# Kernel tuning notes

Hardware: AMD Instinct MI355X
Metric: run time of the kernel (lower is better)

## Reference

```python
import jax, jax.numpy as jnp
import numpy as np

B, N, D = 4, 2048, 1024

def setup_inputs() -> dict:
    key = jax.random.key(0)
    ks = jax.random.split(key, 8)
    s = 1.0 / np.sqrt(D)
    return {
        "x": jax.random.normal(ks[0], (B, N, D), dtype=jnp.float32),
        "Wq": jax.random.normal(ks[1], (D, D), dtype=jnp.float32) * s,
        "bq": jnp.zeros((D,), dtype=jnp.float32),
        "Wk": jax.random.normal(ks[2], (D, D), dtype=jnp.float32) * s,
        "bk": jnp.zeros((D,), dtype=jnp.float32),
        "Wv": jax.random.normal(ks[3], (D, D), dtype=jnp.float32) * s,
        "bv": jnp.zeros((D,), dtype=jnp.float32),
        "gamma": jnp.ones((1,), dtype=jnp.float32),
    }

def reference(x, Wq, bq, Wk, bk, Wv, bv, gamma):
    d = x.shape[-1]
    delta = 1.0 / jnp.sqrt(jnp.asarray(d, dtype=x.dtype))
    # torch Linear: y = x @ W.T + b, W is [out, in]
    Q = jnp.einsum('bnd,ed->bne', x, Wq) + bq
    K = jnp.einsum('bnd,ed->bne', x, Wk) + bk
    V = jnp.einsum('bnd,ed->bne', x, Wv) + bv
    scores = jnp.einsum('bne,bme->bnm', Q, K) * delta  # [B, N, N]
    attn = jax.nn.softmax(scores, axis=-1)
    out = jnp.einsum('bnm,bme->bne', attn, V)
    return out * gamma + x
```

## Files before the change

kernel.cpp:

```cpp
#include <hip/hip_runtime.h>

typedef _Float16 f16;
typedef __attribute__((ext_vector_type(4))) _Float16 f16x4;
typedef __attribute__((ext_vector_type(8))) _Float16 f16x8;
typedef __attribute__((ext_vector_type(4))) float f32x4;

#define B_ 4
#define N_ 2048
#define D_ 1024

__global__ __launch_bounds__(256) void k_cast_all(const float4* __restrict__ x,
                                                  const float4* __restrict__ wq,
                                                  const float4* __restrict__ wk,
                                                  const float4* __restrict__ wv,
                                                  f16x4* __restrict__ xo,
                                                  f16x4* __restrict__ wqo,
                                                  f16x4* __restrict__ wko,
                                                  f16x4* __restrict__ wvo) {
  int b = blockIdx.x;
  const float4* in;
  f16x4* out;
  int idx;
  if (b < 8192)       { in = x;  out = xo;  idx = b * 256 + threadIdx.x; }
  else if (b < 9216)  { in = wq; out = wqo; idx = (b - 8192) * 256 + threadIdx.x; }
  else if (b < 10240) { in = wk; out = wko; idx = (b - 9216) * 256 + threadIdx.x; }
  else                { in = wv; out = wvo; idx = (b - 10240) * 256 + threadIdx.x; }
  float4 v = in[idx];
  f16x4 o = { (_Float16)v.x, (_Float16)v.y, (_Float16)v.z, (_Float16)v.w };
  out[idx] = o;
}

__device__ __forceinline__ void stage_tile(const char* gRowBase, int rowStrideBytes,
                                           int kByte, char* lds, int tid) {
#pragma unroll
  for (int it = 0; it < 4; ++it) {
    int lin = it * 4096 + tid * 16;
    int row = lin >> 7;
    int pchunk = (lin >> 4) & 7;
    int lchunk = pchunk ^ (row & 7);
    const char* g = gRowBase + (long)row * rowStrideBytes + kByte + lchunk * 16;
    char* l = lds + it * 4096 + ((tid >> 6) << 10);
    __builtin_amdgcn_global_load_lds(
        (const __attribute__((address_space(1))) unsigned int*)g,
        (__attribute__((address_space(3))) unsigned int*)l, 16, 0, 0);
  }
}

__device__ __forceinline__ void gemm_mainloop(const f16* __restrict__ A, int lda,
                                              const f16* __restrict__ B, int ldb,
                                              int K, char* ldsA, char* ldsB,
                                              f32x4 acc[4][4]) {
  const int tid = threadIdx.x;
  const int lane = tid & 63, wave = tid >> 6;
  const int wm = wave >> 1, wn = wave & 1;
  const int quad = lane >> 4, l16 = lane & 15;
  const char* Ab = (const char*)A;
  const char* Bb = (const char*)B;
  const int nK = K >> 6;
  for (int ks = 0; ks < nK; ++ks) {
    __syncthreads();
    stage_tile(Ab, lda * 2, ks * 128, ldsA, tid);
    stage_tile(Bb, ldb * 2, ks * 128, ldsB, tid);
    __syncthreads();
#pragma unroll
    for (int kk = 0; kk < 2; ++kk) {
      f16x8 af[4], bfv[4];
#pragma unroll
      for (int i = 0; i < 4; ++i) {
        int c = kk * 4 + quad;
        int rA = wm * 64 + i * 16 + l16;
        af[i] = *(const f16x8*)(ldsA + rA * 128 + ((c ^ (rA & 7)) << 4));
        int rB = wn * 64 + i * 16 + l16;
        bfv[i] = *(const f16x8*)(ldsB + rB * 128 + ((c ^ (rB & 7)) << 4));
      }
#pragma unroll
      for (int i = 0; i < 4; ++i)
#pragma unroll
        for (int j = 0; j < 4; ++j)
          acc[i][j] = __builtin_amdgcn_mfma_f32_16x16x32_f16(af[i], bfv[j], acc[i][j], 0, 0, 0);
    }
  }
}

__global__ __launch_bounds__(256, 2) void k_qkv(const f16* __restrict__ X,
                                                const f16* __restrict__ Wq,
                                                const f16* __restrict__ Wk,
                                                const f16* __restrict__ Wv,
                                                const float* __restrict__ bq,
                                                const float* __restrict__ bk,
                                                const float* __restrict__ bv,
                                                f16* __restrict__ Q, f16* __restrict__ Ko,
                                                f16* __restrict__ V) {
  __shared__ __align__(16) char ldsX[16384];
  __shared__ __align__(16) char ldsW[3][16384];
  int tm = blockIdx.y * 128, tn = blockIdx.x * 128;
  const int tid = threadIdx.x;
  const int lane = tid & 63, wave = tid >> 6;
  const int wm = wave >> 1, wn = wave & 1;
  const int quad = lane >> 4, l16 = lane & 15;
  f32x4 acc[3][4][4];
#pragma unroll
  for (int w = 0; w < 3; ++w)
#pragma unroll
    for (int i = 0; i < 4; ++i)
#pragma unroll
      for (int j = 0; j < 4; ++j) acc[w][i][j] = (f32x4){0.f, 0.f, 0.f, 0.f};

  const char* Xb = (const char*)(X + (long)tm * D_);
  const char* Wb[3] = { (const char*)(Wq + (long)tn * D_),
                        (const char*)(Wk + (long)tn * D_),
                        (const char*)(Wv + (long)tn * D_) };
  for (int ks = 0; ks < (D_ >> 6); ++ks) {
    __syncthreads();
    stage_tile(Xb, D_ * 2, ks * 128, ldsX, tid);
#pragma unroll
    for (int w = 0; w < 3; ++w) stage_tile(Wb[w], D_ * 2, ks * 128, ldsW[w], tid);
    __syncthreads();
#pragma unroll
    for (int kk = 0; kk < 2; ++kk) {
      f16x8 af[4];
#pragma unroll
      for (int i = 0; i < 4; ++i) {
        int c = kk * 4 + quad;
        int rA = wm * 64 + i * 16 + l16;
        af[i] = *(const f16x8*)(ldsX + rA * 128 + ((c ^ (rA & 7)) << 4));
      }
#pragma unroll
      for (int w = 0; w < 3; ++w) {
        f16x8 bfv[4];
#pragma unroll
        for (int j = 0; j < 4; ++j) {
          int c = kk * 4 + quad;
          int rB = wn * 64 + j * 16 + l16;
          bfv[j] = *(const f16x8*)(ldsW[w] + rB * 128 + ((c ^ (rB & 7)) << 4));
        }
#pragma unroll
        for (int i = 0; i < 4; ++i)
#pragma unroll
          for (int j = 0; j < 4; ++j)
            acc[w][i][j] = __builtin_amdgcn_mfma_f32_16x16x32_f16(af[i], bfv[j], acc[w][i][j], 0, 0, 0);
      }
    }
  }

  const float* biases[3] = { bq, bk, bv };
  f16* outs[3] = { Q, Ko, V };
#pragma unroll
  for (int w = 0; w < 3; ++w) {
    f16* out = outs[w];
#pragma unroll
    for (int j = 0; j < 4; ++j) {
      int col = tn + wn * 64 + j * 16 + l16;
      float bb = biases[w][col];
#pragma unroll
      for (int i = 0; i < 4; ++i) {
        int rbase = tm + wm * 64 + i * 16 + quad * 4;
#pragma unroll
        for (int r = 0; r < 4; ++r)
          out[(long)(rbase + r) * D_ + col] = (_Float16)(acc[w][i][j][r] + bb);
      }
    }
  }
}

__global__ __launch_bounds__(256) void k_transpose(const unsigned short* __restrict__ V,
                                                   unsigned short* __restrict__ Vt) {
  __shared__ unsigned short tile[64][68];
  int b = blockIdx.z;
  const unsigned short* in = V + (long)b * N_ * D_;
  unsigned short* outp = Vt + (long)b * D_ * N_;
  int t = threadIdx.x;
  int r = t >> 4;
  int c4 = (t & 15) * 4;
  int mBase = blockIdx.y * 64;
  int eBase = blockIdx.x * 64;
#pragma unroll
  for (int p = 0; p < 4; ++p) {
    int row = p * 16 + r;
    ushort4 v = *(const ushort4*)(in + (long)(mBase + row) * D_ + eBase + c4);
    tile[row][c4 + 0] = v.x; tile[row][c4 + 1] = v.y;
    tile[row][c4 + 2] = v.z; tile[row][c4 + 3] = v.w;
  }
  __syncthreads();
#pragma unroll
  for (int p = 0; p < 4; ++p) {
    int e = p * 16 + r;
    ushort4 v;
    v.x = tile[c4 + 0][e]; v.y = tile[c4 + 1][e];
    v.z = tile[c4 + 2][e]; v.w = tile[c4 + 3][e];
    *(ushort4*)(outp + (long)(eBase + e) * N_ + mBase + c4) = v;
  }
}

__global__ __launch_bounds__(256) void k_scores(const f16* __restrict__ Q,
                                                const f16* __restrict__ Kf,
                                                f16* __restrict__ S) {
  __shared__ __align__(16) char ldsA[16384];
  __shared__ __align__(16) char ldsB[16384];
  int b = blockIdx.z;
  int tm = blockIdx.y * 128, tn = blockIdx.x * 128;
  const f16* A = Q + (long)b * N_ * D_ + (long)tm * D_;
  const f16* Bm = Kf + (long)b * N_ * D_ + (long)tn * D_;
  f32x4 acc[4][4];
#pragma unroll
  for (int i = 0; i < 4; ++i)
#pragma unroll
    for (int j = 0; j < 4; ++j) acc[i][j] = (f32x4){0.f, 0.f, 0.f, 0.f};
  gemm_mainloop(A, D_, Bm, D_, D_, ldsA, ldsB, acc);
  f16* Sb = S + (long)b * N_ * N_;
  const float delta = 0.03125f;
  int tid = threadIdx.x, lane = tid & 63, wave = tid >> 6;
  int wm = wave >> 1, wn = wave & 1, quad = lane >> 4, l16 = lane & 15;
#pragma unroll
  for (int j = 0; j < 4; ++j) {
    int col = tn + wn * 64 + j * 16 + l16;
#pragma unroll
    for (int i = 0; i < 4; ++i) {
      int rbase = tm + wm * 64 + i * 16 + quad * 4;
#pragma unroll
      for (int r = 0; r < 4; ++r)
        Sb[(long)(rbase + r) * N_ + col] = (_Float16)(acc[i][j][r] * delta);
    }
  }
}

__global__ __launch_bounds__(256) void k_softmax(f16* __restrict__ S) {
  f16* row = S + (long)blockIdx.x * 2048;
  int t = threadIdx.x;
  f16x8 v = ((const f16x8*)row)[t];
  float f[8];
#pragma unroll
  for (int i = 0; i < 8; ++i) f[i] = (float)v[i];
  float m = f[0];
#pragma unroll
  for (int i = 1; i < 8; ++i) m = fmaxf(m, f[i]);
#pragma unroll
  for (int off = 32; off > 0; off >>= 1) m = fmaxf(m, __shfl_xor(m, off));
  __shared__ float redm[4], reds[4];
  int wv = t >> 6;
  if ((t & 63) == 0) redm[wv] = m;
  __syncthreads();
  m = fmaxf(fmaxf(redm[0], redm[1]), fmaxf(redm[2], redm[3]));
  float s = 0.f;
#pragma unroll
  for (int i = 0; i < 8; ++i) { f[i] = __expf(f[i] - m); s += f[i]; }
#pragma unroll
  for (int off = 32; off > 0; off >>= 1) s += __shfl_xor(s, off);
  if ((t & 63) == 0) reds[wv] = s;
  __syncthreads();
  s = (reds[0] + reds[1]) + (reds[2] + reds[3]);
  float inv = 1.0f / s;
  f16x8 p;
#pragma unroll
  for (int i = 0; i < 8; ++i) p[i] = (_Float16)(f[i] * inv);
  ((f16x8*)row)[t] = p;
}

__global__ __launch_bounds__(256) void k_out(const f16* __restrict__ P,
                                             const f16* __restrict__ Vt,
                                             const float* __restrict__ x,
                                             const float* __restrict__ gamma,
                                             float* __restrict__ out) {
  __shared__ __align__(16) char ldsA[16384];
  __shared__ __align__(16) char ldsB[16384];
  int b = blockIdx.z;
  int tm = blockIdx.y * 128, tn = blockIdx.x * 128;
  const f16* A = P + (long)b * N_ * N_ + (long)tm * N_;
  const f16* Bm = Vt + (long)b * D_ * N_ + (long)tn * N_;
  f32x4 acc[4][4];
#pragma unroll
  for (int i = 0; i < 4; ++i)
#pragma unroll
    for (int j = 0; j < 4; ++j) acc[i][j] = (f32x4){0.f, 0.f, 0.f, 0.f};
  gemm_mainloop(A, N_, Bm, N_, N_, ldsA, ldsB, acc);
  float g = gamma[0];
  int tid = threadIdx.x, lane = tid & 63, wave = tid >> 6;
  int wm = wave >> 1, wn = wave & 1, quad = lane >> 4, l16 = lane & 15;
#pragma unroll
  for (int j = 0; j < 4; ++j) {
    int col = tn + wn * 64 + j * 16 + l16;
#pragma unroll
    for (int i = 0; i < 4; ++i) {
      int rbase = tm + wm * 64 + i * 16 + quad * 4;
#pragma unroll
      for (int r = 0; r < 4; ++r) {
        long idx = (long)b * N_ * D_ + (long)(rbase + r) * D_ + col;
        out[idx] = acc[i][j][r] * g + x[idx];
      }
    }
  }
}

extern "C" void kernel_launch(void* const* d_in, const int* in_sizes, int n_in,
                              void* d_out, int out_size, void* d_ws, size_t ws_size,
                              hipStream_t stream) {
  const float* x  = (const float*)d_in[0];
  const float* Wq = (const float*)d_in[1];
  const float* bq = (const float*)d_in[2];
  const float* Wk = (const float*)d_in[3];
  const float* bk = (const float*)d_in[4];
  const float* Wv = (const float*)d_in[5];
  const float* bv = (const float*)d_in[6];
  const float* gamma = (const float*)d_in[7];
  float* out = (float*)d_out;
  char* ws = (char*)d_ws;

  f16* Qb  = (f16*)(ws);
  f16* Kb  = (f16*)(ws + (16u << 20));
  f16* Vt  = (f16*)(ws + (32u << 20));
  f16* Xb  = (f16*)(ws + (48u << 20));
  f16* Wqb = (f16*)(ws + (64u << 20));
  f16* Wkb = (f16*)(ws + (66u << 20));
  f16* Wvb = (f16*)(ws + (68u << 20));
  f16* Vb  = (f16*)(ws + (70u << 20));
  f16* S   = (f16*)(ws + (48u << 20));

  k_cast_all<<<11264, 256, 0, stream>>>((const float4*)x, (const float4*)Wq,
                                        (const float4*)Wk, (const float4*)Wv,
                                        (f16x4*)Xb, (f16x4*)Wqb, (f16x4*)Wkb, (f16x4*)Wvb);

  k_qkv<<<dim3(8, 64), 256, 0, stream>>>(Xb, Wqb, Wkb, Wvb, bq, bk, bv, Qb, Kb, Vb);
  k_transpose<<<dim3(16, 32, 4), 256, 0, stream>>>((const unsigned short*)Vb,
                                                   (unsigned short*)Vt);
  k_scores<<<dim3(16, 16, 4), 256, 0, stream>>>(Qb, Kb, S);
  k_softmax<<<8192, 256, 0, stream>>>(S);
  k_out<<<dim3(8, 16, 4), 256, 0, stream>>>(S, Vt, x, gamma, out);
}
```

Measured before the change: 272.2 us.

## Fuse softmax exponent into scores epilogue and V transpose into QKV epilogue

Scores kernel now writes exp(score) directly and accumulates per-row sums via atomics into a zeroed buffer; output GEMM divides by the row sum, eliminating the separate softmax pass over S. The V transpose kernel is removed by writing V transposed through LDS in the QKV epilogue. Dropping max subtraction risks overflow for large-magnitude scores, and atomics add contention.

```diff
diff --git a/kernel.cpp b/kernel.cpp
--- a/kernel.cpp
+++ b/kernel.cpp
@@ -16,8 +16,13 @@
                                                   f16x4* __restrict__ xo,
                                                   f16x4* __restrict__ wqo,
                                                   f16x4* __restrict__ wko,
-                                                  f16x4* __restrict__ wvo) {
+                                                  f16x4* __restrict__ wvo,
+                                                  float* __restrict__ rowsum) {
   int b = blockIdx.x;
+  if (b >= 11264) {
+    rowsum[(b - 11264) * 256 + threadIdx.x] = 0.f;
+    return;
+  }
   const float4* in;
   f16x4* out;
   int idx;
@@ -90,9 +95,9 @@
                                                 const float* __restrict__ bk,
                                                 const float* __restrict__ bv,
                                                 f16* __restrict__ Q, f16* __restrict__ Ko,
-                                                f16* __restrict__ V) {
-  __shared__ __align__(16) char ldsX[16384];
-  __shared__ __align__(16) char ldsW[3][16384];
+                                                f16* __restrict__ Vt) {
+  __shared__ __align__(16) char lds[65536];
+  char* ldsX = lds;
   int tm = blockIdx.y * 128, tn = blockIdx.x * 128;
   const int tid = threadIdx.x;
   const int lane = tid & 63, wave = tid >> 6;
@@ -114,7 +119,7 @@
     __syncthreads();
     stage_tile(Xb, D_ * 2, ks * 128, ldsX, tid);
 #pragma unroll
-    for (int w = 0; w < 3; ++w) stage_tile(Wb[w], D_ * 2, ks * 128, ldsW[w], tid);
+    for (int w = 0; w < 3; ++w) stage_tile(Wb[w], D_ * 2, ks * 128, lds + 16384 * (w + 1), tid);
     __syncthreads();
 #pragma unroll
     for (int kk = 0; kk < 2; ++kk) {
@@ -132,7 +137,7 @@
         for (int j = 0; j < 4; ++j) {
           int c = kk * 4 + quad;
           int rB = wn * 64 + j * 16 + l16;
-          bfv[j] = *(const f16x8*)(ldsW[w] + rB * 128 + ((c ^ (rB & 7)) << 4));
+          bfv[j] = *(const f16x8*)(lds + 16384 * (w + 1) + rB * 128 + ((c ^ (rB & 7)) << 4));
         }
 #pragma unroll
         for (int i = 0; i < 4; ++i)
@@ -143,10 +148,10 @@
     }
   }
 
-  const float* biases[3] = { bq, bk, bv };
-  f16* outs[3] = { Q, Ko, V };
-#pragma unroll
-  for (int w = 0; w < 3; ++w) {
+  const float* biases[2] = { bq, bk };
+  f16* outs[2] = { Q, Ko };
+#pragma unroll
+  for (int w = 0; w < 2; ++w) {
     f16* out = outs[w];
 #pragma unroll
     for (int j = 0; j < 4; ++j) {
@@ -161,40 +166,37 @@
       }
     }
   }
-}
-
-__global__ __launch_bounds__(256) void k_transpose(const unsigned short* __restrict__ V,
-                                                   unsigned short* __restrict__ Vt) {
-  __shared__ unsigned short tile[64][68];
-  int b = blockIdx.z;
-  const unsigned short* in = V + (long)b * N_ * D_;
-  unsigned short* outp = Vt + (long)b * D_ * N_;
-  int t = threadIdx.x;
-  int r = t >> 4;
-  int c4 = (t & 15) * 4;
-  int mBase = blockIdx.y * 64;
-  int eBase = blockIdx.x * 64;
-#pragma unroll
-  for (int p = 0; p < 4; ++p) {
-    int row = p * 16 + r;
-    ushort4 v = *(const ushort4*)(in + (long)(mBase + row) * D_ + eBase + c4);
-    tile[row][c4 + 0] = v.x; tile[row][c4 + 1] = v.y;
-    tile[row][c4 + 2] = v.z; tile[row][c4 + 3] = v.w;
-  }
+
   __syncthreads();
-#pragma unroll
-  for (int p = 0; p < 4; ++p) {
-    int e = p * 16 + r;
-    ushort4 v;
-    v.x = tile[c4 + 0][e]; v.y = tile[c4 + 1][e];
-    v.z = tile[c4 + 2][e]; v.w = tile[c4 + 3][e];
-    *(ushort4*)(outp + (long)(eBase + e) * N_ + mBase + c4) = v;
+  f16* ldsT = (f16*)lds;
+#pragma unroll
+  for (int j = 0; j < 4; ++j) {
+    int cl = wn * 64 + j * 16 + l16;
+    float bb = bv[tn + cl];
+#pragma unroll
+    for (int i = 0; i < 4; ++i) {
+      int rl = wm * 64 + i * 16 + quad * 4;
+      f16x4 p = { (_Float16)(acc[2][i][j][0] + bb), (_Float16)(acc[2][i][j][1] + bb),
+                  (_Float16)(acc[2][i][j][2] + bb), (_Float16)(acc[2][i][j][3] + bb) };
+      *(f16x4*)(ldsT + cl * 136 + rl) = p;
+    }
+  }
+  __syncthreads();
+  int bb_ = tm >> 11, nbase = tm & 2047;
+  f16* VtB = Vt + (long)bb_ * D_ * N_ + nbase;
+#pragma unroll
+  for (int it = 0; it < 8; ++it) {
+    int f = it * 16 + (tid >> 4);
+    int c = tid & 15;
+    f16x8 v = *(const f16x8*)(ldsT + f * 136 + c * 8);
+    *(f16x8*)(VtB + (long)(tn + f) * N_ + c * 8) = v;
   }
 }
 
 __global__ __launch_bounds__(256) void k_scores(const f16* __restrict__ Q,
                                                 const f16* __restrict__ Kf,
-                                                f16* __restrict__ S) {
+                                                f16* __restrict__ S,
+                                                float* __restrict__ rowsum) {
   __shared__ __align__(16) char ldsA[16384];
   __shared__ __align__(16) char ldsB[16384];
   int b = blockIdx.z;
@@ -211,6 +213,11 @@
   const float delta = 0.03125f;
   int tid = threadIdx.x, lane = tid & 63, wave = tid >> 6;
   int wm = wave >> 1, wn = wave & 1, quad = lane >> 4, l16 = lane & 15;
+  float rsum[4][4];
+#pragma unroll
+  for (int i = 0; i < 4; ++i)
+#pragma unroll
+    for (int r = 0; r < 4; ++r) rsum[i][r] = 0.f;
 #pragma unroll
   for (int j = 0; j < 4; ++j) {
     int col = tn + wn * 64 + j * 16 + l16;
@@ -218,48 +225,34 @@
     for (int i = 0; i < 4; ++i) {
       int rbase = tm + wm * 64 + i * 16 + quad * 4;
 #pragma unroll
+      for (int r = 0; r < 4; ++r) {
+        float e = __expf(acc[i][j][r] * delta);
+        Sb[(long)(rbase + r) * N_ + col] = (_Float16)e;
+        rsum[i][r] += e;
+      }
+    }
+  }
+#pragma unroll
+  for (int m = 1; m < 16; m <<= 1)
+#pragma unroll
+    for (int i = 0; i < 4; ++i)
+#pragma unroll
+      for (int r = 0; r < 4; ++r) rsum[i][r] += __shfl_xor(rsum[i][r], m);
+  if (l16 == 0) {
+    float* rs = rowsum + (long)b * N_ + tm;
+#pragma unroll
+    for (int i = 0; i < 4; ++i)
+#pragma unroll
       for (int r = 0; r < 4; ++r)
-        Sb[(long)(rbase + r) * N_ + col] = (_Float16)(acc[i][j][r] * delta);
-    }
-  }
-}
-
-__global__ __launch_bounds__(256) void k_softmax(f16* __restrict__ S) {
-  f16* row = S + (long)blockIdx.x * 2048;
-  int t = threadIdx.x;
-  f16x8 v = ((const f16x8*)row)[t];
-  float f[8];
-#pragma unroll
-  for (int i = 0; i < 8; ++i) f[i] = (float)v[i];
-  float m = f[0];
-#pragma unroll
-  for (int i = 1; i < 8; ++i) m = fmaxf(m, f[i]);
-#pragma unroll
-  for (int off = 32; off > 0; off >>= 1) m = fmaxf(m, __shfl_xor(m, off));
-  __shared__ float redm[4], reds[4];
-  int wv = t >> 6;
-  if ((t & 63) == 0) redm[wv] = m;
-  __syncthreads();
-  m = fmaxf(fmaxf(redm[0], redm[1]), fmaxf(redm[2], redm[3]));
-  float s = 0.f;
-#pragma unroll
-  for (int i = 0; i < 8; ++i) { f[i] = __expf(f[i] - m); s += f[i]; }
-#pragma unroll
-  for (int off = 32; off > 0; off >>= 1) s += __shfl_xor(s, off);
-  if ((t & 63) == 0) reds[wv] = s;
-  __syncthreads();
-  s = (reds[0] + reds[1]) + (reds[2] + reds[3]);
-  float inv = 1.0f / s;
-  f16x8 p;
-#pragma unroll
-  for (int i = 0; i < 8; ++i) p[i] = (_Float16)(f[i] * inv);
-  ((f16x8*)row)[t] = p;
+        atomicAdd(rs + wm * 64 + i * 16 + quad * 4 + r, rsum[i][r]);
+  }
 }
 
 __global__ __launch_bounds__(256) void k_out(const f16* __restrict__ P,
                                              const f16* __restrict__ Vt,
                                              const float* __restrict__ x,
                                              const float* __restrict__ gamma,
+                                             const float* __restrict__ rowsum,
                                              float* __restrict__ out) {
   __shared__ __align__(16) char ldsA[16384];
   __shared__ __align__(16) char ldsB[16384];
@@ -276,6 +269,12 @@
   float g = gamma[0];
   int tid = threadIdx.x, lane = tid & 63, wave = tid >> 6;
   int wm = wave >> 1, wn = wave & 1, quad = lane >> 4, l16 = lane & 15;
+  float inv[4][4];
+#pragma unroll
+  for (int i = 0; i < 4; ++i)
+#pragma unroll
+    for (int r = 0; r < 4; ++r)
+      inv[i][r] = g / rowsum[(long)b * N_ + tm + wm * 64 + i * 16 + quad * 4 + r];
 #pragma unroll
   for (int j = 0; j < 4; ++j) {
     int col = tn + wn * 64 + j * 16 + l16;
@@ -285,7 +284,7 @@
 #pragma unroll
       for (int r = 0; r < 4; ++r) {
         long idx = (long)b * N_ * D_ + (long)(rbase + r) * D_ + col;
-        out[idx] = acc[i][j][r] * g + x[idx];
+        out[idx] = acc[i][j][r] * inv[i][r] + x[idx];
       }
     }
   }
@@ -312,17 +311,14 @@
   f16* Wqb = (f16*)(ws + (64u << 20));
   f16* Wkb = (f16*)(ws + (66u << 20));
   f16* Wvb = (f16*)(ws + (68u << 20));
-  f16* Vb  = (f16*)(ws + (70u << 20));
   f16* S   = (f16*)(ws + (48u << 20));
-
-  k_cast_all<<<11264, 256, 0, stream>>>((const float4*)x, (const float4*)Wq,
+  float* rowsum = (float*)(ws + (80u << 20));
+
+  k_cast_all<<<11296, 256, 0, stream>>>((const float4*)x, (const float4*)Wq,
                                         (const float4*)Wk, (const float4*)Wv,
-                                        (f16x4*)Xb, (f16x4*)Wqb, (f16x4*)Wkb, (f16x4*)Wvb);
-
-  k_qkv<<<dim3(8, 64), 256, 0, stream>>>(Xb, Wqb, Wkb, Wvb, bq, bk, bv, Qb, Kb, Vb);
-  k_transpose<<<dim3(16, 32, 4), 256, 0, stream>>>((const unsigned short*)Vb,
-                                                   (unsigned short*)Vt);
-  k_scores<<<dim3(16, 16, 4), 256, 0, stream>>>(Qb, Kb, S);
-  k_softmax<<<8192, 256, 0, stream>>>(S);
-  k_out<<<dim3(8, 16, 4), 256, 0, stream>>>(S, Vt, x, gamma, out);
-}
+                                        (f16x4*)Xb, (f16x4*)Wqb, (f16x4*)Wkb, (f16x4*)Wvb,
+                                        rowsum);
+  k_qkv<<<dim3(8, 64), 256, 0, stream>>>(Xb, Wqb, Wkb, Wvb, bq, bk, bv, Qb, Kb, Vt);
+  k_scores<<<dim3(16, 16, 4), 256, 0, stream>>>(Qb, Kb, S, rowsum);
+  k_out<<<dim3(8, 16, 4), 256, 0, stream>>>(S, Vt, x, gamma, rowsum, out);
+}
```

Measured after the change: 269.4 us. No clear change (-1.0%).
